# Kernel optimization log

Hardware: AMD Instinct MI355X
Metric: run time of the kernel (lower is better)

The kernel has to match this reference:

```python
import jax, jax.numpy as jnp
import numpy as np

STRIDE = (2, 2)
PADDING = (1, 1)
DILATION = (1, 1)
KERNEL = (3, 3)


def _out_hw(h_in, w_in):
    h_out = (h_in + 2 * PADDING[0] - DILATION[0] * (KERNEL[0] - 1) - 1) // STRIDE[0] + 1
    w_out = (w_in + 2 * PADDING[1] - DILATION[1] * (KERNEL[1] - 1) - 1) // STRIDE[1] + 1
    return h_out, w_out


def _stride_permutation(h_out, w_out):
    # Single-shot multiplexing row permutation (mirrors _get_stride_permutation).
    s_h, s_w = STRIDE
    if s_h == 1 and s_w == 1:
        return np.arange(h_out * w_out)
    perm = []
    for si in range(s_h):
        for sj in range(s_w):
            for i in range((h_out + s_h - 1) // s_h):
                ai = i * s_h + si
                if ai >= h_out:
                    continue
                for j in range((w_out + s_w - 1) // s_w):
                    aj = j * s_w + sj
                    if aj >= w_out:
                        continue
                    perm.append(ai * w_out + aj)
    return np.asarray(perm, dtype=np.int32)


def setup_inputs() -> dict:
    key = jax.random.key(0)
    kx, kw, kb = jax.random.split(key, 3)
    x = jax.random.normal(kx, (16, 256, 64, 64), dtype=jnp.float32)
    weight = jax.random.normal(kw, (256, 256, 3, 3), dtype=jnp.float32)
    bias = jax.random.normal(kb, (256,), dtype=jnp.float32)
    return {"x": x, "weight": weight, "bias": bias}


def reference(x, weight, bias):
    # Toeplitz matrix-vector product == grouped strided conv.
    out = jax.lax.conv_general_dilated(
        x, weight,
        window_strides=STRIDE,
        padding=[(PADDING[0], PADDING[0]), (PADDING[1], PADDING[1])],
        rhs_dilation=DILATION,
        dimension_numbers=("NCHW", "OIHW", "NCHW"),
        feature_group_count=1,
    )  # [B, Cout, h_out, w_out]
    b, c, h_out, w_out = out.shape
    perm = jnp.asarray(_stride_permutation(h_out, w_out))
    flat = out.reshape(b, c, h_out * w_out)
    # permuted[new_idx] = flat[perm[new_idx]] (single-shot stride multiplexing)
    permuted = flat[:, :, perm]
    return permuted + bias[None, :, None]
```

## Files before the change

### kernel.cpp

```cpp
#include <hip/hip_runtime.h>
#include <cstdint>

typedef __attribute__((ext_vector_type(8))) __bf16 bf16x8;
typedef __attribute__((ext_vector_type(4))) float f32x4;

#define NB   16
#define CIN  256
#define COUT 256
#define HIN  64
#define WIN  64
#define HP   66
#define WP   66
#define KTOT 2304
#define XPAD_ELEMS (NB*HP*WP*CIN)

__device__ __forceinline__ uint16_t f2bf(float f) {
  uint32_t u = __builtin_bit_cast(uint32_t, f);
  u = (u + 0x7FFFu + ((u >> 16) & 1u)) >> 16;
  return (uint16_t)u;
}

__global__ void xpose_kernel(const float* __restrict__ x, uint16_t* __restrict__ xpad) {
  __shared__ uint16_t t[64 * 68];
  const int tid = threadIdx.x;
  const int cb = blockIdx.x & 3;
  const int h  = (blockIdx.x >> 2) & 63;
  const int b  = blockIdx.x >> 8;
  const int c0 = cb * 64;
  const float* src = x + (((size_t)(b * 256 + c0) * 64 + h) * 64);
  const int w4 = (tid & 15) * 4;
  #pragma unroll
  for (int it = 0; it < 4; ++it) {
    const int cc = it * 16 + (tid >> 4);
    f32x4 v = *(const f32x4*)(src + cc * 4096 + w4);
    t[(w4 + 0) * 68 + cc] = f2bf(v.x);
    t[(w4 + 1) * 68 + cc] = f2bf(v.y);
    t[(w4 + 2) * 68 + cc] = f2bf(v.z);
    t[(w4 + 3) * 68 + cc] = f2bf(v.w);
  }
  __syncthreads();
  uint16_t* dstbase = xpad + ((size_t)(b * HP + h + 1) * WP + 1) * 256 + c0;
  #pragma unroll
  for (int it = 0; it < 4; ++it) {
    const int slot = it * 256 + tid;
    const int w = slot >> 4, c4 = slot & 15;
    const uint32_t* s2 = (const uint32_t*)&t[w * 68 + c4 * 4];
    uint32_t* d2 = (uint32_t*)(dstbase + w * 256 + c4 * 4);
    d2[0] = s2[0];
    d2[1] = s2[1];
  }
}

__global__ void wprep_kernel(const float* __restrict__ w, uint16_t* __restrict__ bw) {
  const int o = blockIdx.x * 256 + threadIdx.x;
  const int co = o / KTOT;
  const int r  = o - co * KTOT;
  const int tap = r >> 8;
  const int ci  = r & 255;
  bw[o] = f2bf(w[(co * 256 + ci) * 9 + tap]);
}

__device__ __forceinline__ void gl_lds16(const void* g, void* l) {
  __builtin_amdgcn_global_load_lds(
      (__attribute__((address_space(1))) void*)(uintptr_t)g,
      (__attribute__((address_space(3))) void*)(uint32_t)(uintptr_t)l,
      16, 0, 0);
}

__global__ __launch_bounds__(256, 2) void gemm_kernel(
    const uint16_t* __restrict__ xpad, const uint16_t* __restrict__ bw,
    const float* __restrict__ bias, float* __restrict__ out) {
  __shared__ uint16_t lA[128 * 64];
  __shared__ uint16_t lB[64 * 64];
  const int tid = threadIdx.x;
  const int wv = tid >> 6, lane = tid & 63;
  const int quad = lane >> 4, l15 = lane & 15, l7 = lane & 7;
  const int ntile = blockIdx.x & 3;
  const int mtile = blockIdx.x >> 2;
  const int n0 = ntile * 64;
  const int m0 = mtile * 128;
  const int bidx = m0 >> 10;
  const int q0 = m0 & 1023;

  int a_goff[4];
  #pragma unroll
  for (int t = 0; t < 4; ++t) {
    const int slot = t * 256 + tid;
    const int row = slot >> 3;
    const int ch = (slot & 7) ^ (row & 7);
    const int p = q0 + row;
    const int oh = 2 * ((p >> 4) & 15) + ((p >> 9) & 1);
    const int ow = 2 * (p & 15) + ((p >> 8) & 1);
    a_goff[t] = ((bidx * HP + 2 * oh) * WP + 2 * ow) * 256 + ch * 8;
  }
  int b_goff[2];
  #pragma unroll
  for (int t = 0; t < 2; ++t) {
    const int slot = t * 256 + tid;
    const int n = slot >> 3;
    const int kc = (slot & 7) ^ (n & 7);
    b_goff[t] = (n0 + n) * KTOT + kc * 8;
  }

  int aoff[2][2], boff[4][2];
  #pragma unroll
  for (int r = 0; r < 2; ++r)
    #pragma unroll
    for (int s = 0; s < 2; ++s)
      aoff[r][s] = (wv * 32 + r * 16 + l15) * 128 + (((s * 4 + quad) ^ l7) * 16);
  #pragma unroll
  for (int c = 0; c < 4; ++c)
    #pragma unroll
    for (int s = 0; s < 2; ++s)
      boff[c][s] = (c * 16 + l15) * 128 + (((s * 4 + quad) ^ l7) * 16);

  f32x4 acc[2][4];
  #pragma unroll
  for (int r = 0; r < 2; ++r)
    #pragma unroll
    for (int c = 0; c < 4; ++c)
      acc[r][c] = (f32x4){0.f, 0.f, 0.f, 0.f};

  char* lAc = (char*)lA;
  char* lBc = (char*)lB;

  for (int tap = 0; tap < 9; ++tap) {
    const int kh = tap / 3, kw = tap - kh * 3;
    const uint16_t* aptr = xpad + (kh * WP + kw) * 256;
    const uint16_t* bptr = bw + tap * 256;
    for (int ci0 = 0; ci0 < 256; ci0 += 64) {
      __syncthreads();
      #pragma unroll
      for (int t = 0; t < 4; ++t)
        gl_lds16(aptr + a_goff[t] + ci0, lAc + (t * 256 + wv * 64) * 16);
      #pragma unroll
      for (int t = 0; t < 2; ++t)
        gl_lds16(bptr + b_goff[t] + ci0, lBc + (t * 256 + wv * 64) * 16);
      __syncthreads();
      #pragma unroll
      for (int s = 0; s < 2; ++s) {
        bf16x8 af[2], bfr[4];
        #pragma unroll
        for (int r = 0; r < 2; ++r) af[r] = *(const bf16x8*)(lAc + aoff[r][s]);
        #pragma unroll
        for (int c = 0; c < 4; ++c) bfr[c] = *(const bf16x8*)(lBc + boff[c][s]);
        #pragma unroll
        for (int r = 0; r < 2; ++r)
          #pragma unroll
          for (int c = 0; c < 4; ++c)
            acc[r][c] = __builtin_amdgcn_mfma_f32_16x16x32_bf16(af[r], bfr[c], acc[r][c], 0, 0, 0);
      }
    }
  }

  float* obase = out + (size_t)bidx * (COUT * 1024);
  #pragma unroll
  for (int c = 0; c < 4; ++c) {
    const int co = n0 + c * 16 + l15;
    const float bv = bias[co];
    #pragma unroll
    for (int r = 0; r < 2; ++r) {
      const int q = q0 + wv * 32 + r * 16 + quad * 4;
      f32x4 v = acc[r][c];
      v += bv;
      *(f32x4*)(obase + co * 1024 + q) = v;
    }
  }
}

extern "C" void kernel_launch(void* const* d_in, const int* in_sizes, int n_in,
                              void* d_out, int out_size, void* d_ws, size_t ws_size,
                              hipStream_t stream) {
  const float* x    = (const float*)d_in[0];
  const float* w    = (const float*)d_in[1];
  const float* bias = (const float*)d_in[2];
  float* out = (float*)d_out;
  uint16_t* xpad = (uint16_t*)d_ws;
  uint16_t* bwq  = xpad + XPAD_ELEMS;

  hipMemsetAsync(xpad, 0, (size_t)XPAD_ELEMS * sizeof(uint16_t), stream);
  xpose_kernel<<<dim3(16 * 64 * 4), dim3(256), 0, stream>>>(x, xpad);
  wprep_kernel<<<dim3(KTOT), dim3(256), 0, stream>>>(w, bwq);
  gemm_kernel<<<dim3(512), dim3(256), 0, stream>>>(xpad, bwq, bias, out);
}
```

Before: 156.3 us.

## Double-buffer GEMM LDS, zero only pad border, vectorize prep kernels, XCD-aware tile mapping

```diff
diff --git a/kernel.cpp b/kernel.cpp
--- a/kernel.cpp
+++ b/kernel.cpp
@@ -3,16 +3,16 @@
 
 typedef __attribute__((ext_vector_type(8))) __bf16 bf16x8;
 typedef __attribute__((ext_vector_type(4))) float f32x4;
+typedef __attribute__((ext_vector_type(4))) uint32_t u32x4;
 
 #define NB   16
 #define CIN  256
 #define COUT 256
-#define HIN  64
-#define WIN  64
 #define HP   66
 #define WP   66
 #define KTOT 2304
-#define XPAD_ELEMS (NB*HP*WP*CIN)
+#define XPB  (HP*WP*256)
+#define XPAD_ELEMS (NB*XPB)
 
 __device__ __forceinline__ uint16_t f2bf(float f) {
   uint32_t u = __builtin_bit_cast(uint32_t, f);
@@ -20,44 +20,62 @@
   return (uint16_t)u;
 }
 
+__global__ void border_kernel(uint16_t* __restrict__ xpad) {
+  const int idx = blockIdx.x * 256 + threadIdx.x;
+  const int b = idx / 16640;
+  const int r = idx - b * 16640;
+  uint64_t* base = (uint64_t*)(xpad + (size_t)b * XPB);
+  int off;
+  if (r < 4224) {
+    off = r;
+  } else if (r < 8448) {
+    off = 274560 + (r - 4224);
+  } else if (r < 12544) {
+    const int i = r - 8448;
+    off = (1 + (i >> 6)) * 4224 + (i & 63);
+  } else {
+    const int i = r - 12544;
+    off = (1 + (i >> 6)) * 4224 + 4160 + (i & 63);
+  }
+  base[off] = 0;
+}
+
 __global__ void xpose_kernel(const float* __restrict__ x, uint16_t* __restrict__ xpad) {
-  __shared__ uint16_t t[64 * 68];
-  const int tid = threadIdx.x;
-  const int cb = blockIdx.x & 3;
-  const int h  = (blockIdx.x >> 2) & 63;
-  const int b  = blockIdx.x >> 8;
-  const int c0 = cb * 64;
-  const float* src = x + (((size_t)(b * 256 + c0) * 64 + h) * 64);
-  const int w4 = (tid & 15) * 4;
-  #pragma unroll
-  for (int it = 0; it < 4; ++it) {
-    const int cc = it * 16 + (tid >> 4);
-    f32x4 v = *(const f32x4*)(src + cc * 4096 + w4);
-    t[(w4 + 0) * 68 + cc] = f2bf(v.x);
-    t[(w4 + 1) * 68 + cc] = f2bf(v.y);
-    t[(w4 + 2) * 68 + cc] = f2bf(v.z);
-    t[(w4 + 3) * 68 + cc] = f2bf(v.w);
-  }
-  __syncthreads();
-  uint16_t* dstbase = xpad + ((size_t)(b * HP + h + 1) * WP + 1) * 256 + c0;
-  #pragma unroll
-  for (int it = 0; it < 4; ++it) {
-    const int slot = it * 256 + tid;
-    const int w = slot >> 4, c4 = slot & 15;
-    const uint32_t* s2 = (const uint32_t*)&t[w * 68 + c4 * 4];
-    uint32_t* d2 = (uint32_t*)(dstbase + w * 256 + c4 * 4);
-    d2[0] = s2[0];
-    d2[1] = s2[1];
+  const int lane = threadIdx.x & 63;
+  const int wv = threadIdx.x >> 6;
+  const int chalf = blockIdx.x & 1;
+  const int h = (blockIdx.x >> 1) & 63;
+  const int b = blockIdx.x >> 7;
+  const int c0 = chalf * 128 + wv * 32;
+  const float* src = x + ((size_t)(b * 256 + c0) * 64 + h) * 64 + lane;
+  uint16_t* dst = xpad + ((size_t)(b * HP + h + 1) * WP + lane + 1) * 256 + c0;
+  #pragma unroll
+  for (int g = 0; g < 4; ++g) {
+    u32x4 d;
+    #pragma unroll
+    for (int k = 0; k < 4; ++k) {
+      const float v0 = src[(size_t)(g * 8 + 2 * k + 0) * 4096];
+      const float v1 = src[(size_t)(g * 8 + 2 * k + 1) * 4096];
+      d[k] = (uint32_t)f2bf(v0) | ((uint32_t)f2bf(v1) << 16);
+    }
+    *(u32x4*)(dst + g * 8) = d;
   }
 }
 
 __global__ void wprep_kernel(const float* __restrict__ w, uint16_t* __restrict__ bw) {
-  const int o = blockIdx.x * 256 + threadIdx.x;
-  const int co = o / KTOT;
-  const int r  = o - co * KTOT;
-  const int tap = r >> 8;
-  const int ci  = r & 255;
-  bw[o] = f2bf(w[(co * 256 + ci) * 9 + tap]);
+  const int gid = blockIdx.x * 256 + threadIdx.x;
+  const int co = gid / 288;
+  const int r = gid - co * 288;
+  const int tap = r >> 5;
+  const int ci0 = (r & 31) * 8;
+  u32x4 d;
+  #pragma unroll
+  for (int k = 0; k < 4; ++k) {
+    const float v0 = w[((co * 256 + ci0 + 2 * k + 0) * 9) + tap];
+    const float v1 = w[((co * 256 + ci0 + 2 * k + 1) * 9) + tap];
+    d[k] = (uint32_t)f2bf(v0) | ((uint32_t)f2bf(v1) << 16);
+  }
+  *(u32x4*)(bw + co * KTOT + tap * 256 + ci0) = d;
 }
 
 __device__ __forceinline__ void gl_lds16(const void* g, void* l) {
@@ -67,90 +85,100 @@
       16, 0, 0);
 }
 
-__global__ __launch_bounds__(256, 2) void gemm_kernel(
+__global__ __launch_bounds__(128, 2) void gemm_kernel(
     const uint16_t* __restrict__ xpad, const uint16_t* __restrict__ bw,
     const float* __restrict__ bias, float* __restrict__ out) {
-  __shared__ uint16_t lA[128 * 64];
-  __shared__ uint16_t lB[64 * 64];
+  __shared__ uint16_t lA[2][128 * 64];
+  __shared__ uint16_t lB[2][64 * 64];
   const int tid = threadIdx.x;
   const int wv = tid >> 6, lane = tid & 63;
   const int quad = lane >> 4, l15 = lane & 15, l7 = lane & 7;
-  const int ntile = blockIdx.x & 3;
-  const int mtile = blockIdx.x >> 2;
+
+  const int xcd = blockIdx.x & 7;
+  const int grp = blockIdx.x >> 3;
+  const int mtile = (xcd << 4) + (grp >> 2);
+  const int ntile = grp & 3;
   const int n0 = ntile * 64;
   const int m0 = mtile * 128;
   const int bidx = m0 >> 10;
   const int q0 = m0 & 1023;
 
-  int a_goff[4];
-  #pragma unroll
-  for (int t = 0; t < 4; ++t) {
-    const int slot = t * 256 + tid;
-    const int row = slot >> 3;
-    const int ch = (slot & 7) ^ (row & 7);
+  int a_goff[8];
+  #pragma unroll
+  for (int t = 0; t < 8; ++t) {
+    const int c = t * 128 + tid;
+    const int row = c >> 3;
+    const int kc = (c & 7) ^ (row & 7);
     const int p = q0 + row;
     const int oh = 2 * ((p >> 4) & 15) + ((p >> 9) & 1);
     const int ow = 2 * (p & 15) + ((p >> 8) & 1);
-    a_goff[t] = ((bidx * HP + 2 * oh) * WP + 2 * ow) * 256 + ch * 8;
-  }
-  int b_goff[2];
-  #pragma unroll
-  for (int t = 0; t < 2; ++t) {
-    const int slot = t * 256 + tid;
-    const int n = slot >> 3;
-    const int kc = (slot & 7) ^ (n & 7);
+    a_goff[t] = ((bidx * HP + 2 * oh) * WP + 2 * ow) * 256 + kc * 8;
+  }
+  int b_goff[4];
+  #pragma unroll
+  for (int t = 0; t < 4; ++t) {
+    const int c = t * 128 + tid;
+    const int n = c >> 3;
+    const int kc = (c & 7) ^ (n & 7);
     b_goff[t] = (n0 + n) * KTOT + kc * 8;
   }
 
-  int aoff[2][2], boff[4][2];
-  #pragma unroll
-  for (int r = 0; r < 2; ++r)
+  int aoff[4][2], boff[4][2];
+  #pragma unroll
+  for (int r = 0; r < 4; ++r)
     #pragma unroll
     for (int s = 0; s < 2; ++s)
-      aoff[r][s] = (wv * 32 + r * 16 + l15) * 128 + (((s * 4 + quad) ^ l7) * 16);
+      aoff[r][s] = (wv * 64 + r * 16 + l15) * 128 + (((s * 4 + quad) ^ l7) * 16);
   #pragma unroll
   for (int c = 0; c < 4; ++c)
     #pragma unroll
     for (int s = 0; s < 2; ++s)
       boff[c][s] = (c * 16 + l15) * 128 + (((s * 4 + quad) ^ l7) * 16);
 
-  f32x4 acc[2][4];
-  #pragma unroll
-  for (int r = 0; r < 2; ++r)
+  f32x4 acc[4][4];
+  #pragma unroll
+  for (int r = 0; r < 4; ++r)
     #pragma unroll
     for (int c = 0; c < 4; ++c)
       acc[r][c] = (f32x4){0.f, 0.f, 0.f, 0.f};
 
-  char* lAc = (char*)lA;
-  char* lBc = (char*)lB;
-
-  for (int tap = 0; tap < 9; ++tap) {
+  auto stage = [&](int it, int buf) {
+    const int tap = it >> 2;
     const int kh = tap / 3, kw = tap - kh * 3;
-    const uint16_t* aptr = xpad + (kh * WP + kw) * 256;
-    const uint16_t* bptr = bw + tap * 256;
-    for (int ci0 = 0; ci0 < 256; ci0 += 64) {
-      __syncthreads();
+    const int ci0 = (it & 3) << 6;
+    const uint16_t* aptr = xpad + (kh * WP + kw) * 256 + ci0;
+    const uint16_t* bptr = bw + tap * 256 + ci0;
+    char* la = (char*)&lA[buf][0];
+    char* lb = (char*)&lB[buf][0];
+    #pragma unroll
+    for (int t = 0; t < 8; ++t)
+      gl_lds16(aptr + a_goff[t], la + (t * 128 + wv * 64) * 16);
+    #pragma unroll
+    for (int t = 0; t < 4; ++t)
+      gl_lds16(bptr + b_goff[t], lb + (t * 128 + wv * 64) * 16);
+  };
+
+  stage(0, 0);
+  int buf = 0;
+  for (int it = 0; it < 36; ++it) {
+    __syncthreads();
+    if (it < 35) stage(it + 1, buf ^ 1);
+    const char* la = (const char*)&lA[buf][0];
+    const char* lb = (const char*)&lB[buf][0];
+    #pragma unroll
+    for (int s = 0; s < 2; ++s) {
+      bf16x8 af[4], bfr[4];
       #pragma unroll
-      for (int t = 0; t < 4; ++t)
-        gl_lds16(aptr + a_goff[t] + ci0, lAc + (t * 256 + wv * 64) * 16);
+      for (int r = 0; r < 4; ++r) af[r] = *(const bf16x8*)(la + aoff[r][s]);
       #pragma unroll
-      for (int t = 0; t < 2; ++t)
-        gl_lds16(bptr + b_goff[t] + ci0, lBc + (t * 256 + wv * 64) * 16);
-      __syncthreads();
+      for (int c = 0; c < 4; ++c) bfr[c] = *(const bf16x8*)(lb + boff[c][s]);
       #pragma unroll
-      for (int s = 0; s < 2; ++s) {
-        bf16x8 af[2], bfr[4];
+      for (int r = 0; r < 4; ++r)
         #pragma unroll
-        for (int r = 0; r < 2; ++r) af[r] = *(const bf16x8*)(lAc + aoff[r][s]);
-        #pragma unroll
-        for (int c = 0; c < 4; ++c) bfr[c] = *(const bf16x8*)(lBc + boff[c][s]);
-        #pragma unroll
-        for (int r = 0; r < 2; ++r)
-          #pragma unroll
-          for (int c = 0; c < 4; ++c)
-            acc[r][c] = __builtin_amdgcn_mfma_f32_16x16x32_bf16(af[r], bfr[c], acc[r][c], 0, 0, 0);
-      }
+        for (int c = 0; c < 4; ++c)
+          acc[r][c] = __builtin_amdgcn_mfma_f32_16x16x32_bf16(af[r], bfr[c], acc[r][c], 0, 0, 0);
     }
+    buf ^= 1;
   }
 
   float* obase = out + (size_t)bidx * (COUT * 1024);
@@ -159,11 +187,11 @@
     const int co = n0 + c * 16 + l15;
     const float bv = bias[co];
     #pragma unroll
-    for (int r = 0; r < 2; ++r) {
-      const int q = q0 + wv * 32 + r * 16 + quad * 4;
+    for (int r = 0; r < 4; ++r) {
+      const int q = q0 + wv * 64 + r * 16 + quad * 4;
       f32x4 v = acc[r][c];
       v += bv;
-      *(f32x4*)(obase + co * 1024 + q) = v;
+      *(f32x4*)(obase + (size_t)co * 1024 + q) = v;
     }
   }
 }
@@ -178,8 +206,8 @@
   uint16_t* xpad = (uint16_t*)d_ws;
   uint16_t* bwq  = xpad + XPAD_ELEMS;
 
-  hipMemsetAsync(xpad, 0, (size_t)XPAD_ELEMS * sizeof(uint16_t), stream);
-  xpose_kernel<<<dim3(16 * 64 * 4), dim3(256), 0, stream>>>(x, xpad);
-  wprep_kernel<<<dim3(KTOT), dim3(256), 0, stream>>>(w, bwq);
-  gemm_kernel<<<dim3(512), dim3(256), 0, stream>>>(xpad, bwq, bias, out);
-}
+  border_kernel<<<dim3(1040), dim3(256), 0, stream>>>(xpad);
+  xpose_kernel<<<dim3(2048), dim3(256), 0, stream>>>(x, xpad);
+  wprep_kernel<<<dim3(288), dim3(256), 0, stream>>>(w, bwq);
+  gemm_kernel<<<dim3(512), dim3(128), 0, stream>>>(xpad, bwq, bias, out);
+}
```

New measurement: 150.7 us. 1.04x faster.
